# Kernel tuning notes

Measured on AMD Instinct MI355X. Metric: run time of the kernel, lower is better.

Reference implementation:

```python
import jax, jax.numpy as jnp
import numpy as np

NUM_HEADS = 12
HEAD_DIM = 64
DIM = 768
ATTN_DIM = 768
SEQ = 4096


def _rotate_half(t):
    # split last dim in halves: (x1, x2) -> (-x2, x1)
    x1, x2 = jnp.split(t, 2, axis=-1)
    return jnp.concatenate([-x2, x1], axis=-1)


def _apply_rope(t, freqs):
    # t: [B,H,L,d], freqs: [1,1,L,d]
    return t * jnp.cos(freqs) + _rotate_half(t) * jnp.sin(freqs)


def setup_inputs() -> dict:
    key = jax.random.key(0)
    ks = jax.random.split(key, 8)
    x = jax.random.normal(ks[0], (1, SEQ, DIM), dtype=jnp.float32)
    # standard rotary frequencies: theta = pos * inv_freq, concatenated twice to head_dim
    inv_freq = 1.0 / (10000.0 ** (jnp.arange(0, HEAD_DIM, 2, dtype=jnp.float32) / HEAD_DIM))
    pos = jnp.arange(SEQ, dtype=jnp.float32)
    ang = pos[:, None] * inv_freq[None, :]                      # [L, d/2]
    rope = jnp.concatenate([ang, ang], axis=-1)[None, None]     # [1,1,L,d]
    s = 0.02
    Wq = jax.random.normal(ks[1], (ATTN_DIM, DIM), dtype=jnp.float32) * s
    Wk = jax.random.normal(ks[2], (ATTN_DIM, DIM), dtype=jnp.float32) * s
    Wv = jax.random.normal(ks[3], (ATTN_DIM, DIM), dtype=jnp.float32) * s
    Wo = jax.random.normal(ks[4], (DIM, ATTN_DIM), dtype=jnp.float32) * s
    bo = jnp.zeros((DIM,), dtype=jnp.float32)
    gamma = jnp.ones((DIM,), dtype=jnp.float32)
    beta = jnp.zeros((DIM,), dtype=jnp.float32)
    return {"x": x, "Wq": Wq, "Wk": Wk, "Wv": Wv, "Wo": Wo, "bo": bo,
            "gamma": gamma, "beta": beta, "rope": rope}


def reference(x, Wq, Wk, Wv, Wo, bo, gamma, beta, rope):
    B, L, D = x.shape
    residual = x
    # pre-LayerNorm
    mu = jnp.mean(x, axis=-1, keepdims=True)
    var = jnp.mean((x - mu) ** 2, axis=-1, keepdims=True)
    xn = (x - mu) * jax.lax.rsqrt(var + 1e-5) * gamma + beta

    def heads(t):  # [B,L,attn_dim] -> [B,H,L,d]
        return t.reshape(B, L, NUM_HEADS, HEAD_DIM).transpose(0, 2, 1, 3)

    q = heads(xn @ Wq.T)
    k = heads(xn @ Wk.T)
    v = heads(xn @ Wv.T)
    q = _apply_rope(q, rope)
    k = _apply_rope(k, rope)
    v = _apply_rope(v, rope)

    scale = HEAD_DIM ** -0.5
    dots = jnp.einsum('bhid,bhjd->bhij', q, k) * scale
    # causal mask: positions j > i masked
    i = jnp.arange(L)
    mask = i[:, None] < i[None, :]  # True where future
    neg = -jnp.finfo(dots.dtype).max
    dots = jnp.where(mask[None, None], neg, dots)
    attn_map = jax.nn.softmax(dots, axis=-1)

    o = jnp.einsum('bhij,bhjd->bhid', attn_map, v)
    o = o.transpose(0, 2, 1, 3).reshape(B, L, ATTN_DIM)
    out = o @ Wo.T + bo + residual
    return out, attn_map, dots
```

## Files before the change

kernel.cpp:

```cpp
#include <hip/hip_runtime.h>
#include <hip/hip_bf16.h>
#include <cfloat>
#include <cmath>

#define SEQ 4096
#define DIM 768
#define NH 12
#define HD 64
#define NEG_MASK (-0x1.FEp+127f)

typedef __attribute__((ext_vector_type(8))) short short8_t;
typedef __attribute__((ext_vector_type(4))) float f32x4;

static __device__ __forceinline__ unsigned short f2bf(float f) {
  __hip_bfloat16 h = __float2bfloat16(f);
  unsigned short u;
  __builtin_memcpy(&u, &h, 2);
  return u;
}

__global__ __launch_bounds__(256) void ln_kernel(const float* __restrict__ x,
    const float* __restrict__ gamma, const float* __restrict__ beta,
    unsigned short* __restrict__ xnb) {
  int row = blockIdx.x;
  const float* xr = x + (size_t)row * DIM;
  int t = threadIdx.x;
  float v0 = xr[t], v1 = xr[t + 256], v2 = xr[t + 512];
  float s = v0 + v1 + v2;
  float s2 = v0 * v0 + v1 * v1 + v2 * v2;
  for (int off = 32; off > 0; off >>= 1) {
    s += __shfl_down(s, off, 64);
    s2 += __shfl_down(s2, off, 64);
  }
  __shared__ float red[2][4];
  int wid = t >> 6;
  if ((t & 63) == 0) { red[0][wid] = s; red[1][wid] = s2; }
  __syncthreads();
  s = red[0][0] + red[0][1] + red[0][2] + red[0][3];
  s2 = red[1][0] + red[1][1] + red[1][2] + red[1][3];
  float mu = s * (1.0f / DIM);
  float var = s2 * (1.0f / DIM) - mu * mu;
  float rstd = rsqrtf(var + 1e-5f);
  unsigned short* xo = xnb + (size_t)row * DIM;
  xo[t]       = f2bf((v0 - mu) * rstd * gamma[t]       + beta[t]);
  xo[t + 256] = f2bf((v1 - mu) * rstd * gamma[t + 256] + beta[t + 256]);
  xo[t + 512] = f2bf((v2 - mu) * rstd * gamma[t + 512] + beta[t + 512]);
}

__global__ __launch_bounds__(256) void wcvt_kernel(const float* __restrict__ w0,
    const float* __restrict__ w1, const float* __restrict__ w2, const float* __restrict__ w3,
    unsigned short* __restrict__ o0, unsigned short* __restrict__ o1,
    unsigned short* __restrict__ o2, unsigned short* __restrict__ o3) {
  const float* src; unsigned short* dst;
  switch (blockIdx.y) {
    case 0: src = w0; dst = o0; break;
    case 1: src = w1; dst = o1; break;
    case 2: src = w2; dst = o2; break;
    default: src = w3; dst = o3; break;
  }
  size_t base = ((size_t)blockIdx.x * 256 + threadIdx.x) * 8;
  float4 a = *(const float4*)(src + base);
  float4 b = *(const float4*)(src + base + 4);
  ushort4 ua, ub;
  ua.x = f2bf(a.x); ua.y = f2bf(a.y); ua.z = f2bf(a.z); ua.w = f2bf(a.w);
  ub.x = f2bf(b.x); ub.y = f2bf(b.y); ub.z = f2bf(b.z); ub.w = f2bf(b.w);
  *(ushort4*)(dst + base) = ua;
  *(ushort4*)(dst + base + 4) = ub;
}

__global__ __launch_bounds__(256) void qkv_kernel(const unsigned short* __restrict__ xnb,
    const unsigned short* __restrict__ wqb, const unsigned short* __restrict__ wkb,
    const unsigned short* __restrict__ wvb, const float* __restrict__ ropes,
    unsigned short* __restrict__ qb, unsigned short* __restrict__ kb,
    unsigned short* __restrict__ vbT) {
  int z = blockIdx.z;
  const unsigned short* W = (z == 0) ? wqb : (z == 1) ? wkb : wvb;
  int h = blockIdx.y;
  int n0 = h * 64;
  int tid = threadIdx.x;
  int w = tid >> 6, l = tid & 63;
  int col_l = l & 15, rowg = l >> 4, kgrp = rowg * 8;
  int mbase = blockIdx.x * 64 + w * 16;

  f32x4 acc[4];
  #pragma unroll
  for (int g = 0; g < 4; g++) acc[g] = (f32x4){0.f, 0.f, 0.f, 0.f};

  for (int k0 = 0; k0 < DIM; k0 += 32) {
    short8_t a = *(const short8_t*)(xnb + (size_t)(mbase + col_l) * DIM + k0 + kgrp);
    #pragma unroll
    for (int g = 0; g < 4; g++) {
      short8_t bw = *(const short8_t*)(W + (size_t)(n0 + g * 16 + col_l) * DIM + k0 + kgrp);
      acc[g] = __builtin_amdgcn_mfma_f32_16x16x32_bf16(a, bw, acc[g], 0, 0, 0);
    }
  }

  float res[4][4];
  #pragma unroll
  for (int g = 0; g < 4; g++) {
    int d = g * 16 + col_l;
    #pragma unroll
    for (int r = 0; r < 4; r++) {
      int m = mbase + rowg * 4 + r;
      float f = ropes[(size_t)m * HD + d];
      float val = acc[g][r];
      float oth = acc[g ^ 2][r];
      float rot = (g < 2) ? -oth : oth;
      res[g][r] = val * cosf(f) + rot * sinf(f);
    }
  }

  if (z < 2) {
    unsigned short* dst = (z == 0) ? qb : kb;
    #pragma unroll
    for (int g = 0; g < 4; g++) {
      int d = g * 16 + col_l;
      #pragma unroll
      for (int r = 0; r < 4; r++)
        dst[((size_t)h * SEQ + mbase + rowg * 4 + r) * HD + d] = f2bf(res[g][r]);
    }
  } else {
    #pragma unroll
    for (int g = 0; g < 4; g++) {
      int d = g * 16 + col_l;
      ushort4 u;
      u.x = f2bf(res[g][0]); u.y = f2bf(res[g][1]);
      u.z = f2bf(res[g][2]); u.w = f2bf(res[g][3]);
      *(ushort4*)(vbT + ((size_t)h * HD + d) * SEQ + mbase + rowg * 4) = u;
    }
  }
}

__global__ __launch_bounds__(256) void attn_fused(
    const unsigned short* __restrict__ qb, const unsigned short* __restrict__ kb,
    const unsigned short* __restrict__ vbT,
    float* __restrict__ dots, float* __restrict__ attnp, unsigned short* __restrict__ ob) {
  int band = blockIdx.x;
  int h = blockIdx.y;
  int i0 = band * 16;
  int jd = i0 >> 6;
  int tid = threadIdx.x;
  int w = tid >> 6, l = tid & 63;
  int col_l = l & 15, rg = l >> 4, kgrp = rg * 8;
  int c4 = col_l * 4;

  const unsigned short* qh = qb + (size_t)h * SEQ * HD;
  const unsigned short* kh = kb + (size_t)h * SEQ * HD;
  const unsigned short* vh = vbT + (size_t)h * HD * SEQ;
  size_t obase = (size_t)h * SEQ * SEQ;

  __shared__ float pt[4][16][68];
  __shared__ float stats[4][16][2];

  const unsigned short* qrow = qh + (size_t)(i0 + col_l) * HD + kgrp;
  short8_t aq0 = *(const short8_t*)(qrow);
  short8_t aq1 = *(const short8_t*)(qrow + 32);

  float mrow[4], lrow[4];
  #pragma unroll
  for (int r = 0; r < 4; r++) { mrow[r] = -FLT_MAX; lrow[r] = 0.f; }

  for (int jt = w; jt <= jd; jt += 4) {
    int j0 = jt * 64;
    f32x4 acc[4];
    #pragma unroll
    for (int b = 0; b < 4; b++) {
      const unsigned short* kr = kh + (size_t)(j0 + b * 16 + col_l) * HD + kgrp;
      short8_t bk0 = *(const short8_t*)(kr);
      short8_t bk1 = *(const short8_t*)(kr + 32);
      f32x4 z = {0.f, 0.f, 0.f, 0.f};
      acc[b] = __builtin_amdgcn_mfma_f32_16x16x32_bf16(aq0, bk0, z, 0, 0, 0);
      acc[b] = __builtin_amdgcn_mfma_f32_16x16x32_bf16(aq1, bk1, acc[b], 0, 0, 0);
    }
    bool diag = (jt == jd);
    #pragma unroll
    for (int b = 0; b < 4; b++) {
      int j = j0 + b * 16 + col_l;
      #pragma unroll
      for (int r = 0; r < 4; r++) {
        float s = acc[b][r] * 0.125f;
        acc[b][r] = (diag && j > i0 + rg * 4 + r) ? NEG_MASK : s;
      }
    }
    #pragma unroll
    for (int r = 0; r < 4; r++) {
      float tm = fmaxf(fmaxf(acc[0][r], acc[1][r]), fmaxf(acc[2][r], acc[3][r]));
      tm = fmaxf(tm, __shfl_xor(tm, 1, 16));
      tm = fmaxf(tm, __shfl_xor(tm, 2, 16));
      tm = fmaxf(tm, __shfl_xor(tm, 4, 16));
      tm = fmaxf(tm, __shfl_xor(tm, 8, 16));
      float ps = __expf(acc[0][r] - tm) + __expf(acc[1][r] - tm) +
                 __expf(acc[2][r] - tm) + __expf(acc[3][r] - tm);
      ps += __shfl_xor(ps, 1, 16);
      ps += __shfl_xor(ps, 2, 16);
      ps += __shfl_xor(ps, 4, 16);
      ps += __shfl_xor(ps, 8, 16);
      float nm = fmaxf(mrow[r], tm);
      lrow[r] = lrow[r] * __expf(mrow[r] - nm) + ps * __expf(tm - nm);
      mrow[r] = nm;
    }
    #pragma unroll
    for (int b = 0; b < 4; b++)
      #pragma unroll
      for (int r = 0; r < 4; r++)
        pt[w][rg * 4 + r][b * 16 + col_l] = acc[b][r];
    #pragma unroll
    for (int e = 0; e < 4; e++) {
      float4 v = *(const float4*)&pt[w][e * 4 + rg][c4];
      *(float4*)(dots + obase + (size_t)(i0 + e * 4 + rg) * SEQ + j0 + c4) = v;
    }
  }

  if (col_l == 0) {
    #pragma unroll
    for (int r = 0; r < 4; r++) {
      stats[w][rg * 4 + r][0] = mrow[r];
      stats[w][rg * 4 + r][1] = lrow[r];
    }
  }
  __syncthreads();
  float M_[4], rl_[4];
  #pragma unroll
  for (int r = 0; r < 4; r++) {
    int row = rg * 4 + r;
    float m0 = stats[0][row][0], m1 = stats[1][row][0];
    float m2 = stats[2][row][0], m3 = stats[3][row][0];
    float mm = fmaxf(fmaxf(m0, m1), fmaxf(m2, m3));
    float L = stats[0][row][1] * __expf(m0 - mm) + stats[1][row][1] * __expf(m1 - mm) +
              stats[2][row][1] * __expf(m2 - mm) + stats[3][row][1] * __expf(m3 - mm);
    M_[r] = mm;
    rl_[r] = 1.0f / L;
  }

  f32x4 o[4];
  #pragma unroll
  for (int dg = 0; dg < 4; dg++) o[dg] = (f32x4){0.f, 0.f, 0.f, 0.f};

  for (int jt = w; jt <= jd; jt += 4) {
    int j0 = jt * 64;
    f32x4 acc[4];
    #pragma unroll
    for (int b = 0; b < 4; b++) {
      const unsigned short* kr = kh + (size_t)(j0 + b * 16 + col_l) * HD + kgrp;
      short8_t bk0 = *(const short8_t*)(kr);
      short8_t bk1 = *(const short8_t*)(kr + 32);
      f32x4 z = {0.f, 0.f, 0.f, 0.f};
      acc[b] = __builtin_amdgcn_mfma_f32_16x16x32_bf16(aq0, bk0, z, 0, 0, 0);
      acc[b] = __builtin_amdgcn_mfma_f32_16x16x32_bf16(aq1, bk1, acc[b], 0, 0, 0);
    }
    bool diag = (jt == jd);
    #pragma unroll
    for (int b = 0; b < 4; b++) {
      int j = j0 + b * 16 + col_l;
      #pragma unroll
      for (int r = 0; r < 4; r++) {
        float s = acc[b][r] * 0.125f;
        s = (diag && j > i0 + rg * 4 + r) ? NEG_MASK : s;
        float p = __expf(s - M_[r]) * rl_[r];
        pt[w][rg * 4 + r][b * 16 + col_l] = p;
      }
    }
    #pragma unroll
    for (int e = 0; e < 4; e++) {
      float4 v = *(const float4*)&pt[w][e * 4 + rg][c4];
      *(float4*)(attnp + obase + (size_t)(i0 + e * 4 + rg) * SEQ + j0 + c4) = v;
    }
    short8_t pa[2];
    #pragma unroll
    for (int ks = 0; ks < 2; ks++) {
      const float* src = &pt[w][col_l][ks * 32 + kgrp];
      float4 x0 = *(const float4*)src;
      float4 x1 = *(const float4*)(src + 4);
      short8_t t;
      t[0] = (short)f2bf(x0.x); t[1] = (short)f2bf(x0.y);
      t[2] = (short)f2bf(x0.z); t[3] = (short)f2bf(x0.w);
      t[4] = (short)f2bf(x1.x); t[5] = (short)f2bf(x1.y);
      t[6] = (short)f2bf(x1.z); t[7] = (short)f2bf(x1.w);
      pa[ks] = t;
    }
    #pragma unroll
    for (int dg = 0; dg < 4; dg++) {
      const unsigned short* vr = vh + (size_t)(dg * 16 + col_l) * SEQ + j0 + kgrp;
      short8_t bv0 = *(const short8_t*)(vr);
      short8_t bv1 = *(const short8_t*)(vr + 32);
      o[dg] = __builtin_amdgcn_mfma_f32_16x16x32_bf16(pa[0], bv0, o[dg], 0, 0, 0);
      o[dg] = __builtin_amdgcn_mfma_f32_16x16x32_bf16(pa[1], bv1, o[dg], 0, 0, 0);
    }
  }

  {
    int c0 = (jd + 1) * 64;
    int nf4 = (SEQ - c0) >> 2;
    if (nf4 > 0) {
      float4 dm = make_float4(NEG_MASK, NEG_MASK, NEG_MASK, NEG_MASK);
      float4 zz = make_float4(0.f, 0.f, 0.f, 0.f);
      for (int r16 = 0; r16 < 16; r16++) {
        float4* dr = (float4*)(dots  + obase + (size_t)(i0 + r16) * SEQ + c0);
        float4* ar = (float4*)(attnp + obase + (size_t)(i0 + r16) * SEQ + c0);
        for (int c = tid; c < nf4; c += 256) { dr[c] = dm; ar[c] = zz; }
      }
    }
  }

  __syncthreads();
  #pragma unroll
  for (int dg = 0; dg < 4; dg++)
    #pragma unroll
    for (int r = 0; r < 4; r++)
      pt[w][rg * 4 + r][dg * 16 + col_l] = o[dg][r];
  __syncthreads();
  {
    int idx = tid * 4;
    int row = idx >> 6, col = idx & 63;
    float4 s = *(const float4*)&pt[0][row][col];
    #pragma unroll
    for (int w2 = 1; w2 < 4; w2++) {
      float4 t = *(const float4*)&pt[w2][row][col];
      s.x += t.x; s.y += t.y; s.z += t.z; s.w += t.w;
    }
    ushort4 u;
    u.x = f2bf(s.x); u.y = f2bf(s.y); u.z = f2bf(s.z); u.w = f2bf(s.w);
    *(ushort4*)(ob + (size_t)(i0 + row) * DIM + h * HD + col) = u;
  }
}

__global__ __launch_bounds__(256) void out_kernel(const unsigned short* __restrict__ ob,
    const unsigned short* __restrict__ wob, const float* __restrict__ bias,
    const float* __restrict__ resid, float* __restrict__ out) {
  int n0 = blockIdx.y * 64;
  int tid = threadIdx.x;
  int w = tid >> 6, l = tid & 63;
  int col_l = l & 15, rowg = l >> 4, kgrp = rowg * 8;
  int mbase = blockIdx.x * 64 + w * 16;

  f32x4 acc[4];
  #pragma unroll
  for (int g = 0; g < 4; g++) acc[g] = (f32x4){0.f, 0.f, 0.f, 0.f};

  for (int k0 = 0; k0 < DIM; k0 += 32) {
    short8_t a = *(const short8_t*)(ob + (size_t)(mbase + col_l) * DIM + k0 + kgrp);
    #pragma unroll
    for (int g = 0; g < 4; g++) {
      short8_t bw = *(const short8_t*)(wob + (size_t)(n0 + g * 16 + col_l) * DIM + k0 + kgrp);
      acc[g] = __builtin_amdgcn_mfma_f32_16x16x32_bf16(a, bw, acc[g], 0, 0, 0);
    }
  }
  #pragma unroll
  for (int g = 0; g < 4; g++) {
    int n = n0 + g * 16 + col_l;
    float bn = bias[n];
    #pragma unroll
    for (int r = 0; r < 4; r++) {
      int m = mbase + rowg * 4 + r;
      out[(size_t)m * DIM + n] = acc[g][r] + bn + resid[(size_t)m * DIM + n];
    }
  }
}

extern "C" void kernel_launch(void* const* d_in, const int* in_sizes, int n_in,
                              void* d_out, int out_size, void* d_ws, size_t ws_size,
                              hipStream_t stream) {
  const float* x     = (const float*)d_in[0];
  const float* Wq    = (const float*)d_in[1];
  const float* Wk    = (const float*)d_in[2];
  const float* Wv    = (const float*)d_in[3];
  const float* Wo    = (const float*)d_in[4];
  const float* bo    = (const float*)d_in[5];
  const float* gamma = (const float*)d_in[6];
  const float* beta  = (const float*)d_in[7];
  const float* rope  = (const float*)d_in[8];

  float* out  = (float*)d_out;
  float* attn = out + (size_t)SEQ * DIM;
  float* dots = attn + (size_t)NH * SEQ * SEQ;

  char* ws = (char*)d_ws;
  unsigned short* xnb = (unsigned short*)(ws);
  unsigned short* qb  = (unsigned short*)(ws + 6291456);
  unsigned short* kb  = (unsigned short*)(ws + 12582912);
  unsigned short* vbT = (unsigned short*)(ws + 18874368);
  unsigned short* ob  = (unsigned short*)(ws + 25165824);
  unsigned short* wqb = (unsigned short*)(ws + 31457280);
  unsigned short* wkb = (unsigned short*)(ws + 32636928);
  unsigned short* wvb = (unsigned short*)(ws + 33816576);
  unsigned short* wob = (unsigned short*)(ws + 34996224);

  ln_kernel<<<SEQ, 256, 0, stream>>>(x, gamma, beta, xnb);
  wcvt_kernel<<<dim3(288, 4), 256, 0, stream>>>(Wq, Wk, Wv, Wo, wqb, wkb, wvb, wob);
  qkv_kernel<<<dim3(SEQ / 64, NH, 3), 256, 0, stream>>>(xnb, wqb, wkb, wvb, rope, qb, kb, vbT);
  attn_fused<<<dim3(SEQ / 16, NH), 256, 0, stream>>>(qb, kb, vbT, dots, attn, ob);
  out_kernel<<<dim3(SEQ / 64, DIM / 64), 256, 0, stream>>>(ob, wob, bo, x, out);
}
```

Before: 655.6 us.

## Process 32-row bands per block with two wave pairs and lane-local softmax stats

Each attention block now covers 32 query rows. Two groups of two waves split the key tiles between them, where each wave previously took every fourth tile of a 16-row band. The per-tile online softmax keeps per-lane running max and sum and merges them with one shuffle reduction after the loop, which removes the eight shuffles per row per tile. The grid is halved and the masked-tail fill covers 32 rows per block. This cuts per-tile shuffle overhead and launches fewer blocks, at the cost of fewer blocks to balance the causal work.

```diff
diff --git a/kernel.cpp b/kernel.cpp
--- a/kernel.cpp
+++ b/kernel.cpp
@@ -137,12 +137,14 @@
     float* __restrict__ dots, float* __restrict__ attnp, unsigned short* __restrict__ ob) {
   int band = blockIdx.x;
   int h = blockIdx.y;
-  int i0 = band * 16;
+  int i0 = band * 32;
   int jd = i0 >> 6;
   int tid = threadIdx.x;
   int w = tid >> 6, l = tid & 63;
+  int g = w >> 1, sst = w & 1;
   int col_l = l & 15, rg = l >> 4, kgrp = rg * 8;
   int c4 = col_l * 4;
+  int r0 = i0 + g * 16;
 
   const unsigned short* qh = qb + (size_t)h * SEQ * HD;
   const unsigned short* kh = kb + (size_t)h * SEQ * HD;
@@ -152,15 +154,15 @@
   __shared__ float pt[4][16][68];
   __shared__ float stats[4][16][2];
 
-  const unsigned short* qrow = qh + (size_t)(i0 + col_l) * HD + kgrp;
+  const unsigned short* qrow = qh + (size_t)(r0 + col_l) * HD + kgrp;
   short8_t aq0 = *(const short8_t*)(qrow);
   short8_t aq1 = *(const short8_t*)(qrow + 32);
 
-  float mrow[4], lrow[4];
-  #pragma unroll
-  for (int r = 0; r < 4; r++) { mrow[r] = -FLT_MAX; lrow[r] = 0.f; }
-
-  for (int jt = w; jt <= jd; jt += 4) {
+  float mreg[4], lreg[4];
+  #pragma unroll
+  for (int r = 0; r < 4; r++) { mreg[r] = -FLT_MAX; lreg[r] = 0.f; }
+
+  for (int jt = sst; jt <= jd; jt += 2) {
     int j0 = jt * 64;
     f32x4 acc[4];
     #pragma unroll
@@ -179,25 +181,19 @@
       #pragma unroll
       for (int r = 0; r < 4; r++) {
         float s = acc[b][r] * 0.125f;
-        acc[b][r] = (diag && j > i0 + rg * 4 + r) ? NEG_MASK : s;
+        acc[b][r] = (diag && j > r0 + rg * 4 + r) ? NEG_MASK : s;
       }
     }
     #pragma unroll
     for (int r = 0; r < 4; r++) {
       float tm = fmaxf(fmaxf(acc[0][r], acc[1][r]), fmaxf(acc[2][r], acc[3][r]));
-      tm = fmaxf(tm, __shfl_xor(tm, 1, 16));
-      tm = fmaxf(tm, __shfl_xor(tm, 2, 16));
-      tm = fmaxf(tm, __shfl_xor(tm, 4, 16));
-      tm = fmaxf(tm, __shfl_xor(tm, 8, 16));
-      float ps = __expf(acc[0][r] - tm) + __expf(acc[1][r] - tm) +
-                 __expf(acc[2][r] - tm) + __expf(acc[3][r] - tm);
-      ps += __shfl_xor(ps, 1, 16);
-      ps += __shfl_xor(ps, 2, 16);
-      ps += __shfl_xor(ps, 4, 16);
-      ps += __shfl_xor(ps, 8, 16);
-      float nm = fmaxf(mrow[r], tm);
-      lrow[r] = lrow[r] * __expf(mrow[r] - nm) + ps * __expf(tm - nm);
-      mrow[r] = nm;
+      if (tm > -1e30f) {
+        float nm = fmaxf(mreg[r], tm);
+        lreg[r] = lreg[r] * __expf(mreg[r] - nm) +
+                  __expf(acc[0][r] - nm) + __expf(acc[1][r] - nm) +
+                  __expf(acc[2][r] - nm) + __expf(acc[3][r] - nm);
+        mreg[r] = nm;
+      }
     }
     #pragma unroll
     for (int b = 0; b < 4; b++)
@@ -207,15 +203,28 @@
     #pragma unroll
     for (int e = 0; e < 4; e++) {
       float4 v = *(const float4*)&pt[w][e * 4 + rg][c4];
-      *(float4*)(dots + obase + (size_t)(i0 + e * 4 + rg) * SEQ + j0 + c4) = v;
-    }
-  }
-
+      *(float4*)(dots + obase + (size_t)(r0 + e * 4 + rg) * SEQ + j0 + c4) = v;
+    }
+  }
+
+  #pragma unroll
+  for (int r = 0; r < 4; r++) {
+    float m = mreg[r], lv = lreg[r];
+    #pragma unroll
+    for (int off = 1; off < 16; off <<= 1) {
+      float om = __shfl_xor(m, off, 16);
+      float ol = __shfl_xor(lv, off, 16);
+      float nm = fmaxf(m, om);
+      lv = lv * __expf(m - nm) + ol * __expf(om - nm);
+      m = nm;
+    }
+    mreg[r] = m; lreg[r] = lv;
+  }
   if (col_l == 0) {
     #pragma unroll
     for (int r = 0; r < 4; r++) {
-      stats[w][rg * 4 + r][0] = mrow[r];
-      stats[w][rg * 4 + r][1] = lrow[r];
+      stats[w][rg * 4 + r][0] = mreg[r];
+      stats[w][rg * 4 + r][1] = lreg[r];
     }
   }
   __syncthreads();
@@ -223,11 +232,10 @@
   #pragma unroll
   for (int r = 0; r < 4; r++) {
     int row = rg * 4 + r;
-    float m0 = stats[0][row][0], m1 = stats[1][row][0];
-    float m2 = stats[2][row][0], m3 = stats[3][row][0];
-    float mm = fmaxf(fmaxf(m0, m1), fmaxf(m2, m3));
-    float L = stats[0][row][1] * __expf(m0 - mm) + stats[1][row][1] * __expf(m1 - mm) +
-              stats[2][row][1] * __expf(m2 - mm) + stats[3][row][1] * __expf(m3 - mm);
+    float m0 = stats[g * 2][row][0], m1 = stats[g * 2 + 1][row][0];
+    float l0 = stats[g * 2][row][1], l1 = stats[g * 2 + 1][row][1];
+    float mm = fmaxf(m0, m1);
+    float L = l0 * __expf(m0 - mm) + l1 * __expf(m1 - mm);
     M_[r] = mm;
     rl_[r] = 1.0f / L;
   }
@@ -236,7 +244,7 @@
   #pragma unroll
   for (int dg = 0; dg < 4; dg++) o[dg] = (f32x4){0.f, 0.f, 0.f, 0.f};
 
-  for (int jt = w; jt <= jd; jt += 4) {
+  for (int jt = sst; jt <= jd; jt += 2) {
     int j0 = jt * 64;
     f32x4 acc[4];
     #pragma unroll
@@ -255,7 +263,7 @@
       #pragma unroll
       for (int r = 0; r < 4; r++) {
         float s = acc[b][r] * 0.125f;
-        s = (diag && j > i0 + rg * 4 + r) ? NEG_MASK : s;
+        s = (diag && j > r0 + rg * 4 + r) ? NEG_MASK : s;
         float p = __expf(s - M_[r]) * rl_[r];
         pt[w][rg * 4 + r][b * 16 + col_l] = p;
       }
@@ -263,7 +271,7 @@
     #pragma unroll
     for (int e = 0; e < 4; e++) {
       float4 v = *(const float4*)&pt[w][e * 4 + rg][c4];
-      *(float4*)(attnp + obase + (size_t)(i0 + e * 4 + rg) * SEQ + j0 + c4) = v;
+      *(float4*)(attnp + obase + (size_t)(r0 + e * 4 + rg) * SEQ + j0 + c4) = v;
     }
     short8_t pa[2];
     #pragma unroll
@@ -294,9 +302,9 @@
     if (nf4 > 0) {
       float4 dm = make_float4(NEG_MASK, NEG_MASK, NEG_MASK, NEG_MASK);
       float4 zz = make_float4(0.f, 0.f, 0.f, 0.f);
-      for (int r16 = 0; r16 < 16; r16++) {
-        float4* dr = (float4*)(dots  + obase + (size_t)(i0 + r16) * SEQ + c0);
-        float4* ar = (float4*)(attnp + obase + (size_t)(i0 + r16) * SEQ + c0);
+      for (int r32 = 0; r32 < 32; r32++) {
+        float4* dr = (float4*)(dots  + obase + (size_t)(i0 + r32) * SEQ + c0);
+        float4* ar = (float4*)(attnp + obase + (size_t)(i0 + r32) * SEQ + c0);
         for (int c = tid; c < nf4; c += 256) { dr[c] = dm; ar[c] = zz; }
       }
     }
@@ -309,18 +317,17 @@
     for (int r = 0; r < 4; r++)
       pt[w][rg * 4 + r][dg * 16 + col_l] = o[dg][r];
   __syncthreads();
-  {
-    int idx = tid * 4;
-    int row = idx >> 6, col = idx & 63;
-    float4 s = *(const float4*)&pt[0][row][col];
-    #pragma unroll
-    for (int w2 = 1; w2 < 4; w2++) {
-      float4 t = *(const float4*)&pt[w2][row][col];
-      s.x += t.x; s.y += t.y; s.z += t.z; s.w += t.w;
-    }
+  #pragma unroll
+  for (int i = 0; i < 2; i++) {
+    int idx = tid + i * 256;
+    int gg = idx >> 8, rem = idx & 255;
+    int row = rem >> 4, col4 = (rem & 15) * 4;
+    float4 a = *(const float4*)&pt[gg * 2][row][col4];
+    float4 b = *(const float4*)&pt[gg * 2 + 1][row][col4];
     ushort4 u;
-    u.x = f2bf(s.x); u.y = f2bf(s.y); u.z = f2bf(s.z); u.w = f2bf(s.w);
-    *(ushort4*)(ob + (size_t)(i0 + row) * DIM + h * HD + col) = u;
+    u.x = f2bf(a.x + b.x); u.y = f2bf(a.y + b.y);
+    u.z = f2bf(a.z + b.z); u.w = f2bf(a.w + b.w);
+    *(ushort4*)(ob + (size_t)(i0 + gg * 16 + row) * DIM + h * HD + col4) = u;
   }
 }
 
@@ -388,6 +395,6 @@
   ln_kernel<<<SEQ, 256, 0, stream>>>(x, gamma, beta, xnb);
   wcvt_kernel<<<dim3(288, 4), 256, 0, stream>>>(Wq, Wk, Wv, Wo, wqb, wkb, wvb, wob);
   qkv_kernel<<<dim3(SEQ / 64, NH, 3), 256, 0, stream>>>(xnb, wqb, wkb, wvb, rope, qb, kb, vbT);
-  attn_fused<<<dim3(SEQ / 16, NH), 256, 0, stream>>>(qb, kb, vbT, dots, attn, ob);
+  attn_fused<<<dim3(SEQ / 32, NH), 256, 0, stream>>>(qb, kb, vbT, dots, attn, ob);
   out_kernel<<<dim3(SEQ / 64, DIM / 64), 256, 0, stream>>>(ob, wob, bo, x, out);
 }
```

New measurement: 739.6 us. 1.13x slower.
